# Optimization experiments

Hardware: AMD Instinct MI355X
Metric: run time of the kernel (lower is better)

The kernel has to match this reference:

```python
import jax, jax.numpy as jnp
import numpy as np

KERNEL_MUL = 2.0
KERNEL_NUM = 5
EPS = 1e-8


def setup_inputs() -> dict:
    key = jax.random.key(0)
    k1, k2 = jax.random.split(key)
    source = jax.random.normal(k1, (4096, 512), dtype=jnp.float32)
    target = jax.random.normal(k2, (4096, 512), dtype=jnp.float32)
    return {"source": source, "target": target}


def reference(source, target):
    ns = source.shape[0]
    total = jnp.concatenate([source, target], axis=0)          # (N, D)
    n = total.shape[0]
    # Pairwise squared L2 via the matmul identity ||a-b||^2 = ||a||^2 + ||b||^2 - 2 a.b
    sq = jnp.sum(total * total, axis=1)                        # (N,)
    gram = total @ total.T                                     # (N, N)
    l2 = jnp.maximum(sq[:, None] + sq[None, :] - 2.0 * gram, 0.0)
    # Adaptive bandwidth: mean of off-diagonal distances (diagonal is 0)
    bandwidth = jnp.sum(l2) / (n * n - n)
    # Multi-bandwidth RBF kernel sum
    half = KERNEL_NUM // 2
    kernel = jnp.zeros_like(l2)
    for i in range(KERNEL_NUM):
        bw = bandwidth * (KERNEL_MUL ** (i - half))
        kernel = kernel + jnp.exp(-l2 / (bw + EPS))
    xx = jnp.mean(kernel[:ns, :ns])
    yy = jnp.mean(kernel[ns:, ns:])
    xy = jnp.mean(kernel[:ns, ns:])
    return xx + yy - 2.0 * xy
```

## Files before the change

kernel.cpp:

```cpp
#include <hip/hip_runtime.h>
#include <stdint.h>

typedef uint16_t u16;
typedef uint32_t u32;

#define NS 4096
#define NTOT 8192
#define DIM 512
#define NTILE 2080
#define GRID_MMD 1024

typedef __attribute__((ext_vector_type(8))) short bf16x8;
typedef __attribute__((ext_vector_type(4))) float f32x4;

__device__ inline u16 f2bf(float f) {
    u32 u = __float_as_uint(f);
    return (u16)((u + 0x7fffu + ((u >> 16) & 1u)) >> 16);
}

__device__ inline void load_lds16(const void* g, void* l) {
    __builtin_amdgcn_global_load_lds((__attribute__((address_space(1))) void*)g,
                                     (__attribute__((address_space(3))) void*)l,
                                     16, 0, 0);
}


__global__ __launch_bounds__(256) void k_prep(const float* __restrict__ src,
                                              const float* __restrict__ tgt,
                                              u16* __restrict__ Tb,
                                              float* __restrict__ sq,
                                              float* __restrict__ cp) {
    __shared__ u16 xb[2][16][520];
    __shared__ float cs_l[4][DIM];
    const int b = blockIdx.x, tid = threadIdx.x;
    const int w = tid >> 6, lane = tid & 63;
    const int rbl = w >> 1;
    const int i0 = (w & 1) * 8;

    float cs[8];
#pragma unroll
    for (int e = 0; e < 8; ++e) cs[e] = 0.f;

#pragma unroll
    for (int i = 0; i < 8; ++i) {
        const int fr = i0 + i;
        const int r = b * 32 + rbl * 16 + fr;
        const float* rowp = (r < NS) ? (src + (size_t)r * DIM)
                                     : (tgt + (size_t)(r - NS) * DIM);
        float4 v0 = *(const float4*)(rowp + lane * 8);
        float4 v1 = *(const float4*)(rowp + lane * 8 + 4);
        float vx[8] = {v0.x, v0.y, v0.z, v0.w, v1.x, v1.y, v1.z, v1.w};
        float ss = 0.f;
#pragma unroll
        for (int e = 0; e < 8; ++e) { ss += vx[e] * vx[e]; cs[e] += vx[e]; }
        u32 pk[4];
#pragma unroll
        for (int e = 0; e < 4; ++e)
            pk[e] = (u32)f2bf(vx[2 * e]) | ((u32)f2bf(vx[2 * e + 1]) << 16);
        *(uint4*)&xb[rbl][fr][lane * 8] = make_uint4(pk[0], pk[1], pk[2], pk[3]);
#pragma unroll
        for (int off = 32; off; off >>= 1) ss += __shfl_down(ss, off);
        if (lane == 0) sq[r] = ss;
    }
#pragma unroll
    for (int e = 0; e < 8; ++e) cs_l[w][lane * 8 + e] = cs[e];
    __syncthreads();

    const int fq = lane >> 4, frx = lane & 15;
    const int rbg = b * 2 + rbl;
#pragma unroll
    for (int tt = 0; tt < 8; ++tt) {
        const int kt = (w & 1) * 8 + tt;
        uint4 v = *(const uint4*)&xb[rbl][frx][(kt * 4 + fq) * 8];
        *(uint4*)(Tb + (size_t)(rbg * 16 + kt) * 512 + lane * 8) = v;
    }

    float a0 = cs_l[0][tid] + cs_l[1][tid] + cs_l[2][tid] + cs_l[3][tid];
    float a1 = cs_l[0][tid + 256] + cs_l[1][tid + 256] + cs_l[2][tid + 256] + cs_l[3][tid + 256];
    cp[(size_t)b * DIM + tid] = a0;
    cp[(size_t)b * DIM + tid + 256] = a1;
}

__global__ __launch_bounds__(256) void k_band(const float* __restrict__ sq,
                                              const float* __restrict__ cp,
                                              float* __restrict__ scales,
                                              double* __restrict__ accum) {
    __shared__ double red[4];
    const int tid = threadIdx.x;
    const int w = tid >> 6, lane = tid & 63;

    double ssq = 0.0;
    for (int i = tid; i < NTOT; i += 256) ssq += (double)sq[i];

    double s2 = 0.0;
#pragma unroll
    for (int cc = 0; cc < 2; ++cc) {
        const int c = tid + cc * 256;
        float b0 = 0.f, b1 = 0.f, b2 = 0.f, b3 = 0.f;
#pragma unroll 8
        for (int k = 0; k < 256; k += 4) {
            b0 += cp[(size_t)(k + 0) * DIM + c];
            b1 += cp[(size_t)(k + 1) * DIM + c];
            b2 += cp[(size_t)(k + 2) * DIM + c];
            b3 += cp[(size_t)(k + 3) * DIM + c];
        }
        double sc = (double)b0 + (double)b1 + (double)b2 + (double)b3;
        s2 += sc * sc;
    }

    auto blkreduce = [&](double v) -> double {
#pragma unroll
        for (int off = 32; off; off >>= 1) v += __shfl_down(v, off);
        __syncthreads();
        if (lane == 0) red[w] = v;
        __syncthreads();
        return red[0] + red[1] + red[2] + red[3];
    };
    double sumsq = blkreduce(ssq);
    double s2t = blkreduce(s2);

    if (tid < 5) {
        const double nn = (double)NTOT;
        double bw = (2.0 * nn * sumsq - 2.0 * s2t) / (nn * nn - nn);
        const double fac[5] = {0.25, 0.5, 1.0, 2.0, 4.0};
        scales[tid] = (float)(-1.0 / (bw * fac[tid] + 1e-8));
    }
    if (tid == 5) *accum = 0.0;
}

__global__ __launch_bounds__(256) void k_mmd(const u16* __restrict__ Tb,
                                             const float* __restrict__ sq,
                                             const float* __restrict__ scales,
                                             double* __restrict__ accum) {
    __shared__ __align__(16) u16 As[3][4096];
    __shared__ __align__(16) u16 Bs[3][4096];
    __shared__ double red[4];

    const int tid = threadIdx.x;
    const int wid = tid >> 6, lane = tid & 63;
    const int wr = wid >> 1, wc = wid & 1;
    const int fr = lane & 15, fq = lane >> 4;
    const float s2c = scales[2];

    const int b = (int)blockIdx.x;
    const int bp = (b & 7) * (GRID_MMD / 8) + (b >> 3);
    const int lo = (bp * 65) >> 5;
    const int hi = ((bp + 1) * 65) >> 5;

    double lacc_tot = 0.0;

    for (int t = lo; t < hi; ++t) {
        int bi = (int)((sqrtf(8.0f * (float)t + 1.0f) - 1.0f) * 0.5f);
        while ((bi + 1) * (bi + 2) / 2 <= t) ++bi;
        while (bi * (bi + 1) / 2 > t) --bi;
        const int bj = t - bi * (bi + 1) / 2;

        int offA[2], offB[2];
#pragma unroll
        for (int q = 0; q < 2; ++q) {
            offA[q] = (bi * 8 + wid * 2 + q) * 16 * 512 + lane * 8;
            offB[q] = (bj * 8 + wid * 2 + q) * 16 * 512 + lane * 8;
        }

        auto stage = [&](int buf, int kt) {
#pragma unroll
            for (int q = 0; q < 2; ++q) {
                load_lds16(Tb + offA[q] + kt * 512, &As[buf][(wid * 2 + q) * 512]);
                load_lds16(Tb + offB[q] + kt * 512, &Bs[buf][(wid * 2 + q) * 512]);
            }
        };

        f32x4 acc[4][4];
#pragma unroll
        for (int m = 0; m < 4; ++m)
#pragma unroll
            for (int n = 0; n < 4; ++n) acc[m][n] = (f32x4){0.f, 0.f, 0.f, 0.f};

        __builtin_amdgcn_s_barrier();
        asm volatile("" ::: "memory");

        stage(0, 0);
        stage(1, 1);

#pragma unroll
        for (int u = 0; u < 16; ++u) {
            if (u == 15) asm volatile("s_waitcnt vmcnt(0)" ::: "memory");
            else         asm volatile("s_waitcnt vmcnt(4)" ::: "memory");
            __builtin_amdgcn_s_barrier();
            asm volatile("" ::: "memory");

            const u16* Ab = As[u % 3];
            const u16* Bb = Bs[u % 3];
            bf16x8 af[4], bfr[4];
#pragma unroll
            for (int m = 0; m < 4; ++m)
                af[m] = *(const bf16x8*)(Ab + (wr * 4 + m) * 512 + lane * 8);
#pragma unroll
            for (int n = 0; n < 4; ++n)
                bfr[n] = *(const bf16x8*)(Bb + (wc * 4 + n) * 512 + lane * 8);
#pragma unroll
            for (int m = 0; m < 4; ++m)
#pragma unroll
                for (int n = 0; n < 4; ++n)
                    acc[m][n] = __builtin_amdgcn_mfma_f32_16x16x32_bf16(af[m], bfr[n], acc[m][n], 0, 0, 0);

            if (u + 2 < 16) stage((u + 2) % 3, u + 2);
        }

        const int rowA0 = bi * 128, rowB0 = bj * 128;
        float sqc[4];
#pragma unroll
        for (int n = 0; n < 4; ++n) sqc[n] = sq[rowB0 + wc * 64 + n * 16 + fr];

        float facc = 0.f;
#pragma unroll
        for (int m = 0; m < 4; ++m) {
            float4 s4 = *(const float4*)(sq + rowA0 + wr * 64 + m * 16 + fq * 4);
            float sqr[4] = {s4.x, s4.y, s4.z, s4.w};
#pragma unroll
            for (int n = 0; n < 4; ++n) {
#pragma unroll
                for (int r = 0; r < 4; ++r) {
                    float g = acc[m][n][r];
                    float l2 = fmaxf(sqr[r] + sqc[n] - 2.0f * g, 0.0f);
                    float e = __expf(s2c * l2);
                    float e2 = e * e;
                    float e4 = e2 * e2;
                    float r1, r2;
                    asm("v_sqrt_f32 %0, %1" : "=v"(r1) : "v"(e));
                    asm("v_sqrt_f32 %0, %1" : "=v"(r2) : "v"(r1));
                    facc += e4 + e2 + e + r1 + r2;
                }
            }
        }

        const double wfac = ((bi == bj) ? 1.0 : 2.0) *
                            (((bi < 32) == (bj < 32)) ? 1.0 : -1.0);
        lacc_tot += (double)facc * wfac;
    }

    double v = lacc_tot;
#pragma unroll
    for (int off = 32; off; off >>= 1) v += __shfl_down(v, off);
    __syncthreads();
    if (lane == 0) red[wid] = v;
    __syncthreads();
    if (tid == 0)
        atomicAdd(accum, red[0] + red[1] + red[2] + red[3]);
}

__global__ void k_final(const double* __restrict__ accum, float* __restrict__ out) {
    if (threadIdx.x == 0)
        out[0] = (float)(accum[0] / ((double)NS * (double)NS));
}

extern "C" void kernel_launch(void* const* d_in, const int* in_sizes, int n_in,
                              void* d_out, int out_size, void* d_ws, size_t ws_size,
                              hipStream_t stream) {
    const float* src = (const float*)d_in[0];
    const float* tgt = (const float*)d_in[1];
    char* ws = (char*)d_ws;

    const size_t MB8 = 8u * 1024 * 1024;
    u16* Tb       = (u16*)ws;
    float* sq     = (float*)(ws + MB8);
    float* cp     = (float*)(ws + MB8 + 32 * 1024);
    float* scales = (float*)(ws + MB8 + 544 * 1024);
    double* accum = (double*)(ws + MB8 + 544 * 1024 + 64);

    k_prep<<<256, 256, 0, stream>>>(src, tgt, Tb, sq, cp);
    k_band<<<1, 256, 0, stream>>>(sq, cp, scales, accum);
    k_mmd<<<GRID_MMD, 256, 0, stream>>>(Tb, sq, scales, accum);
    k_final<<<1, 64, 0, stream>>>(accum, (float*)d_out);
}
```

Measured before the change: 156.0 us.

## Quantize Gram operands to FP8 and fold final division into MMD kernel

Converts the packed operand matrix from bf16 to fp8 (e4m3), which halves its memory and LDS footprint and computes the Gram tiles with fp8 MFMA instructions over 8 K-steps of 64 instead of 16 steps of 32. The prep kernel's transpose/packing layout is rewritten to match the fp8 fragment layout. The separate final kernel is removed: the last block, found with an atomic counter, writes the output. FP8 quantization of the inputs reduces Gram precision, which risks the MMD value drifting past tolerance because it comes from cancellation between large kernel sums.

```diff
diff --git a/kernel.cpp b/kernel.cpp
--- a/kernel.cpp
+++ b/kernel.cpp
@@ -1,8 +1,10 @@
 #include <hip/hip_runtime.h>
 #include <stdint.h>
 
+typedef uint8_t u8;
 typedef uint16_t u16;
 typedef uint32_t u32;
+typedef unsigned long long u64;
 
 #define NS 4096
 #define NTOT 8192
@@ -10,13 +12,8 @@
 #define NTILE 2080
 #define GRID_MMD 1024
 
-typedef __attribute__((ext_vector_type(8))) short bf16x8;
+typedef __attribute__((ext_vector_type(2))) long l64x2;
 typedef __attribute__((ext_vector_type(4))) float f32x4;
-
-__device__ inline u16 f2bf(float f) {
-    u32 u = __float_as_uint(f);
-    return (u16)((u + 0x7fffu + ((u >> 16) & 1u)) >> 16);
-}
 
 __device__ inline void load_lds16(const void* g, void* l) {
     __builtin_amdgcn_global_load_lds((__attribute__((address_space(1))) void*)g,
@@ -27,10 +24,10 @@
 
 __global__ __launch_bounds__(256) void k_prep(const float* __restrict__ src,
                                               const float* __restrict__ tgt,
-                                              u16* __restrict__ Tb,
+                                              u8* __restrict__ Tb,
                                               float* __restrict__ sq,
                                               float* __restrict__ cp) {
-    __shared__ u16 xb[2][16][520];
+    __shared__ u8 xb[2][16][528];
     __shared__ float cs_l[4][DIM];
     const int b = blockIdx.x, tid = threadIdx.x;
     const int w = tid >> 6, lane = tid & 63;
@@ -53,11 +50,13 @@
         float ss = 0.f;
 #pragma unroll
         for (int e = 0; e < 8; ++e) { ss += vx[e] * vx[e]; cs[e] += vx[e]; }
-        u32 pk[4];
-#pragma unroll
-        for (int e = 0; e < 4; ++e)
-            pk[e] = (u32)f2bf(vx[2 * e]) | ((u32)f2bf(vx[2 * e + 1]) << 16);
-        *(uint4*)&xb[rbl][fr][lane * 8] = make_uint4(pk[0], pk[1], pk[2], pk[3]);
+        int dlo = 0, dhi = 0;
+        dlo = __builtin_amdgcn_cvt_pk_fp8_f32(vx[0], vx[1], dlo, 0);
+        dlo = __builtin_amdgcn_cvt_pk_fp8_f32(vx[2], vx[3], dlo, 1);
+        dhi = __builtin_amdgcn_cvt_pk_fp8_f32(vx[4], vx[5], dhi, 0);
+        dhi = __builtin_amdgcn_cvt_pk_fp8_f32(vx[6], vx[7], dhi, 1);
+        *(u32*)&xb[rbl][fr][lane * 8] = (u32)dlo;
+        *(u32*)&xb[rbl][fr][lane * 8 + 4] = (u32)dhi;
 #pragma unroll
         for (int off = 32; off; off >>= 1) ss += __shfl_down(ss, off);
         if (lane == 0) sq[r] = ss;
@@ -66,13 +65,17 @@
     for (int e = 0; e < 8; ++e) cs_l[w][lane * 8 + e] = cs[e];
     __syncthreads();
 
-    const int fq = lane >> 4, frx = lane & 15;
-    const int rbg = b * 2 + rbl;
-#pragma unroll
-    for (int tt = 0; tt < 8; ++tt) {
-        const int kt = (w & 1) * 8 + tt;
-        uint4 v = *(const uint4*)&xb[rbl][frx][(kt * 4 + fq) * 8];
-        *(uint4*)(Tb + (size_t)(rbg * 16 + kt) * 512 + lane * 8) = v;
+    const int row = lane & 15, oct = lane >> 4;
+#pragma unroll
+    for (int ff = 0; ff < 4; ++ff) {
+        const int f = w * 4 + ff;
+        const int frbl = f >> 3, kt2 = f & 7;
+        u64 a0 = *(const u64*)&xb[frbl][row][kt2 * 64 + oct * 8];
+        u64 a1 = *(const u64*)&xb[frbl][row][kt2 * 64 + 32 + oct * 8];
+        const int rbg = b * 2 + frbl;
+        u8* dst = Tb + (size_t)(rbg * 8 + kt2) * 1024 + lane * 16;
+        *(u64*)dst = a0;
+        *(u64*)(dst + 8) = a1;
     }
 
     float a0 = cs_l[0][tid] + cs_l[1][tid] + cs_l[2][tid] + cs_l[3][tid];
@@ -84,7 +87,8 @@
 __global__ __launch_bounds__(256) void k_band(const float* __restrict__ sq,
                                               const float* __restrict__ cp,
                                               float* __restrict__ scales,
-                                              double* __restrict__ accum) {
+                                              double* __restrict__ accum,
+                                              u32* __restrict__ counter) {
     __shared__ double red[4];
     const int tid = threadIdx.x;
     const int w = tid >> 6, lane = tid & 63;
@@ -126,14 +130,17 @@
         scales[tid] = (float)(-1.0 / (bw * fac[tid] + 1e-8));
     }
     if (tid == 5) *accum = 0.0;
-}
-
-__global__ __launch_bounds__(256) void k_mmd(const u16* __restrict__ Tb,
+    if (tid == 6) *counter = 0u;
+}
+
+__global__ __launch_bounds__(256) void k_mmd(const u8* __restrict__ Tb,
                                              const float* __restrict__ sq,
                                              const float* __restrict__ scales,
-                                             double* __restrict__ accum) {
-    __shared__ __align__(16) u16 As[3][4096];
-    __shared__ __align__(16) u16 Bs[3][4096];
+                                             double* __restrict__ accum,
+                                             u32* __restrict__ counter,
+                                             float* __restrict__ out) {
+    __shared__ __align__(16) u8 As[3][8192];
+    __shared__ __align__(16) u8 Bs[3][8192];
     __shared__ double red[4];
 
     const int tid = threadIdx.x;
@@ -155,18 +162,18 @@
         while (bi * (bi + 1) / 2 > t) --bi;
         const int bj = t - bi * (bi + 1) / 2;
 
-        int offA[2], offB[2];
+        u32 offA[2], offB[2];
 #pragma unroll
         for (int q = 0; q < 2; ++q) {
-            offA[q] = (bi * 8 + wid * 2 + q) * 16 * 512 + lane * 8;
-            offB[q] = (bj * 8 + wid * 2 + q) * 16 * 512 + lane * 8;
-        }
-
-        auto stage = [&](int buf, int kt) {
+            offA[q] = (u32)((bi * 8 + wid * 2 + q) * 8) * 1024 + lane * 16;
+            offB[q] = (u32)((bj * 8 + wid * 2 + q) * 8) * 1024 + lane * 16;
+        }
+
+        auto stage = [&](int buf, int u) {
 #pragma unroll
             for (int q = 0; q < 2; ++q) {
-                load_lds16(Tb + offA[q] + kt * 512, &As[buf][(wid * 2 + q) * 512]);
-                load_lds16(Tb + offB[q] + kt * 512, &Bs[buf][(wid * 2 + q) * 512]);
+                load_lds16(Tb + offA[q] + u * 1024, &As[buf][(wid * 2 + q) * 1024]);
+                load_lds16(Tb + offB[q] + u * 1024, &Bs[buf][(wid * 2 + q) * 1024]);
             }
         };
 
@@ -183,28 +190,32 @@
         stage(1, 1);
 
 #pragma unroll
-        for (int u = 0; u < 16; ++u) {
-            if (u == 15) asm volatile("s_waitcnt vmcnt(0)" ::: "memory");
-            else         asm volatile("s_waitcnt vmcnt(4)" ::: "memory");
+        for (int u = 0; u < 8; ++u) {
+            if (u == 7) asm volatile("s_waitcnt vmcnt(0)" ::: "memory");
+            else        asm volatile("s_waitcnt vmcnt(4)" ::: "memory");
             __builtin_amdgcn_s_barrier();
             asm volatile("" ::: "memory");
 
-            const u16* Ab = As[u % 3];
-            const u16* Bb = Bs[u % 3];
-            bf16x8 af[4], bfr[4];
+            const u8* Ab = As[u % 3];
+            const u8* Bb = Bs[u % 3];
+            l64x2 av[4], bv[4];
 #pragma unroll
             for (int m = 0; m < 4; ++m)
-                af[m] = *(const bf16x8*)(Ab + (wr * 4 + m) * 512 + lane * 8);
+                av[m] = *(const l64x2*)(Ab + (wr * 4 + m) * 1024 + lane * 16);
 #pragma unroll
             for (int n = 0; n < 4; ++n)
-                bfr[n] = *(const bf16x8*)(Bb + (wc * 4 + n) * 512 + lane * 8);
+                bv[n] = *(const l64x2*)(Bb + (wc * 4 + n) * 1024 + lane * 16);
 #pragma unroll
             for (int m = 0; m < 4; ++m)
 #pragma unroll
-                for (int n = 0; n < 4; ++n)
-                    acc[m][n] = __builtin_amdgcn_mfma_f32_16x16x32_bf16(af[m], bfr[n], acc[m][n], 0, 0, 0);
-
-            if (u + 2 < 16) stage((u + 2) % 3, u + 2);
+                for (int n = 0; n < 4; ++n) {
+                    acc[m][n] = __builtin_amdgcn_mfma_f32_16x16x32_fp8_fp8(
+                        av[m].x, bv[n].x, acc[m][n], 0, 0, 0);
+                    acc[m][n] = __builtin_amdgcn_mfma_f32_16x16x32_fp8_fp8(
+                        av[m].y, bv[n].y, acc[m][n], 0, 0, 0);
+                }
+
+            if (u + 2 < 8) stage((u + 2) % 3, u + 2);
         }
 
         const int rowA0 = bi * 128, rowB0 = bj * 128;
@@ -245,13 +256,16 @@
     __syncthreads();
     if (lane == 0) red[wid] = v;
     __syncthreads();
-    if (tid == 0)
+
+    if (tid == 0) {
         atomicAdd(accum, red[0] + red[1] + red[2] + red[3]);
-}
-
-__global__ void k_final(const double* __restrict__ accum, float* __restrict__ out) {
-    if (threadIdx.x == 0)
-        out[0] = (float)(accum[0] / ((double)NS * (double)NS));
+        __threadfence();
+        u32 done = atomicAdd(counter, 1u);
+        if (done == GRID_MMD - 1) {
+            double tot = atomicAdd(accum, 0.0);
+            out[0] = (float)(tot / ((double)NS * (double)NS));
+        }
+    }
 }
 
 extern "C" void kernel_launch(void* const* d_in, const int* in_sizes, int n_in,
@@ -261,15 +275,15 @@
     const float* tgt = (const float*)d_in[1];
     char* ws = (char*)d_ws;
 
-    const size_t MB8 = 8u * 1024 * 1024;
-    u16* Tb       = (u16*)ws;
-    float* sq     = (float*)(ws + MB8);
-    float* cp     = (float*)(ws + MB8 + 32 * 1024);
-    float* scales = (float*)(ws + MB8 + 544 * 1024);
-    double* accum = (double*)(ws + MB8 + 544 * 1024 + 64);
+    const size_t MB4 = 4u * 1024 * 1024;
+    u8* Tb        = (u8*)ws;
+    float* sq     = (float*)(ws + MB4);
+    float* cp     = (float*)(ws + MB4 + 32 * 1024);
+    float* scales = (float*)(ws + MB4 + 544 * 1024);
+    double* accum = (double*)(ws + MB4 + 544 * 1024 + 128);
+    u32* counter  = (u32*)(ws + MB4 + 544 * 1024 + 192);
 
     k_prep<<<256, 256, 0, stream>>>(src, tgt, Tb, sq, cp);
-    k_band<<<1, 256, 0, stream>>>(sq, cp, scales, accum);
-    k_mmd<<<GRID_MMD, 256, 0, stream>>>(Tb, sq, scales, accum);
-    k_final<<<1, 64, 0, stream>>>(accum, (float*)d_out);
-}
+    k_band<<<1, 256, 0, stream>>>(sq, cp, scales, accum, counter);
+    k_mmd<<<GRID_MMD, 256, 0, stream>>>(Tb, sq, scales, accum, counter, (float*)d_out);
+}
```

Result: faster. 146.0 us (-6.4%).
